# Kernel optimization log

Hardware: AMD Instinct MI355X
Metric: run time of the kernel (lower is better)

Reference implementation:

```python
import jax, jax.numpy as jnp
import numpy as np

B = 16384      # rays
H = 128        # field hidden dim


def setup_inputs() -> dict:
    key = jax.random.key(0)
    ks = jax.random.split(key, 8)
    origins = jax.random.normal(ks[0], (B, 3), dtype=jnp.float32)
    directions = jax.random.normal(ks[1], (B, 3), dtype=jnp.float32)
    directions = directions / jnp.linalg.norm(directions, axis=-1, keepdims=True)
    # Field: simple MLP 3 -> H -> H -> 4 (rgb + sigma)
    W1 = jax.random.normal(ks[2], (3, H), dtype=jnp.float32) * (1.0 / np.sqrt(3.0))
    b1 = jnp.zeros((H,), dtype=jnp.float32)
    W2 = jax.random.normal(ks[3], (H, H), dtype=jnp.float32) * (1.0 / np.sqrt(H))
    b2 = jnp.zeros((H,), dtype=jnp.float32)
    W3 = jax.random.normal(ks[4], (H, 4), dtype=jnp.float32) * (1.0 / np.sqrt(H))
    b3 = jnp.zeros((4,), dtype=jnp.float32)
    return {"origins": origins, "directions": directions,
            "W1": W1, "b1": b1, "W2": W2, "b2": b2, "W3": W3, "b3": b3,
            "near": 2, "far": 6, "num_samples": 64}


def _field(x, W1, b1, W2, b2, W3, b3):
    h = jax.nn.relu(x @ W1 + b1)
    h = jax.nn.relu(h @ W2 + b2)
    return h @ W3 + b3


def reference(origins, directions, W1, b1, W2, b2, W3, b3, near, far, num_samples):
    near = jnp.float32(near)
    far = jnp.float32(far)
    # 1. generate_samples: segment boundaries + midpoints along each ray
    depths = jnp.linspace(near, far, num_samples + 1)            # [S+1]
    midpoints = 0.5 * (depths[:-1] + depths[1:])                 # [S]
    # [B, S, 3] = origin + t * direction
    locs = origins[:, None, :] + midpoints[None, :, None] * directions[:, None, :]
    # 2. evaluate field
    f = _field(locs.reshape(-1, 3), W1, b1, W2, b2, W3, b3)
    f = f.reshape(origins.shape[0], num_samples, 4)
    # NOTE: source overwrites the sigmoid'd colors with raw outputs (faithful)
    colors = f[..., :3]                                          # [B, S, 3]
    sigma = f[..., 3]                                            # [B, S]
    # 3. alpha values
    delta = depths[1:] - depths[:-1]                             # [S]
    alphas = 1.0 - jnp.exp(-sigma * delta[None, :])              # [B, S]
    # 4. alpha compositing (black background)
    ones = jnp.ones_like(alphas[:, :1])
    transmittance = jnp.cumprod(jnp.concatenate([ones, 1.0 - alphas], axis=1), axis=1)[:, :-1]
    weights = alphas * transmittance                             # [B, S]
    radiance = jnp.sum(weights[..., None] * colors, axis=1)      # [B, 3]
    return radiance
```

## Files before the change

### kernel.cpp

```cpp
#include <hip/hip_runtime.h>


typedef _Float16 f16;
typedef __attribute__((ext_vector_type(2))) _Float16 h2v;
typedef __attribute__((ext_vector_type(8))) _Float16 half8;
typedef __attribute__((ext_vector_type(4))) float floatx4;

#define H 128
#define NS 64

static __device__ __forceinline__ h2v pkrtz(float a, float b) {
  return __builtin_bit_cast(h2v, __builtin_amdgcn_cvt_pkrtz(a, b));
}

__global__ void nerf_setup(const float* __restrict__ W2, const float* __restrict__ W3,
                           const float* __restrict__ b2,
                           f16* __restrict__ wsW2, f16* __restrict__ wsW3,
                           f16* __restrict__ wsB2) {
  int t = blockIdx.x * blockDim.x + threadIdx.x;
  if (t < 8192) {
    int j2 = t & 3, lane = (t >> 2) & 63, mt = (t >> 8) & 7, ks = t >> 11;
    int l16 = lane & 15;
    int k = ks * 32 + ((lane >> 4) * 8) + 2 * j2;
    int n = 32 * (l16 >> 2) + mt * 4 + (l16 & 3);
    wsW2[2 * t]     = (f16)W2[k * H + n];
    wsW2[2 * t + 1] = (f16)W2[(k + 1) * H + n];
  } else if (t < 9216) {
    int u = t - 8192;
    int j2 = u & 3, lane = (u >> 2) & 63, ks = u >> 8;
    int c = lane & 15;
    int k3 = 32 * (lane >> 4) + ks * 8 + 2 * j2;
    wsW3[2 * u]     = (c < 4) ? (f16)W3[k3 * 4 + c]       : (f16)0.0f;
    wsW3[2 * u + 1] = (c < 4) ? (f16)W3[(k3 + 1) * 4 + c] : (f16)0.0f;
  } else if (t < 9344) {
    int i = t - 9216;
    wsB2[i] = (f16)b2[i];
  }
}

__global__ __launch_bounds__(256, 2) void nerf_main(
    const float* __restrict__ origins, const float* __restrict__ dirs,
    const float* __restrict__ W1, const float* __restrict__ b1,
    const float* __restrict__ b3,
    const f16* __restrict__ wsW2, const f16* __restrict__ wsW3,
    const f16* __restrict__ wsB2,
    float* __restrict__ out)
{
  __shared__ __align__(16) f16   popd[4][2][H];
  __shared__ __align__(16) float f_lds[4][64][4];

  const int t = threadIdx.x;
  const int w = t >> 6, lane = t & 63, quad = lane >> 4, l16 = lane & 15;
  const float delta = 4.0f / NS;
  const int ray = blockIdx.x * 4 + w;

  {
    const float o0 = origins[ray*3], o1 = origins[ray*3+1], o2 = origins[ray*3+2];
    const float d0 = dirs[ray*3],    d1 = dirs[ray*3+1],    d2 = dirs[ray*3+2];
    const int k0 = lane * 2;
    const float2 wr0 = *(const float2*)&W1[0*H + k0];
    const float2 wr1 = *(const float2*)&W1[1*H + k0];
    const float2 wr2 = *(const float2*)&W1[2*H + k0];
    const float2 bb  = *(const float2*)&b1[k0];
    float poa = fmaf(o2, wr2.x, fmaf(o1, wr1.x, fmaf(o0, wr0.x, bb.x)));
    float pob = fmaf(o2, wr2.y, fmaf(o1, wr1.y, fmaf(o0, wr0.y, bb.y)));
    float pda = fmaf(d2, wr2.x, fmaf(d1, wr1.x, d0 * wr0.x));
    float pdb = fmaf(d2, wr2.y, fmaf(d1, wr1.y, d0 * wr0.y));
    h2v po2; po2[0] = (f16)poa; po2[1] = (f16)pob;
    h2v pd2; pd2[0] = (f16)pda; pd2[1] = (f16)pdb;
    *(h2v*)&popd[w][0][k0] = po2;
    *(h2v*)&popd[w][1][k0] = pd2;
  }

  half8 m8[4];
  #pragma unroll
  for (int tr = 0; tr < 4; ++tr)
    m8[tr] = (half8)(f16)(2.0f + (tr*16 + l16 + 0.5f) * delta);

  floatx4 acc[8][4];
  #pragma unroll
  for (int mt = 0; mt < 8; ++mt)
    #pragma unroll
    for (int tr = 0; tr < 4; ++tr) acc[mt][tr] = (floatx4)(0.0f);

  const half8* w2f = (const half8*)wsW2;
  const half8 z8 = (half8)(f16)0.0f;
  half8 awA[8], awB[8];
  #pragma unroll
  for (int mt = 0; mt < 8; ++mt) awA[mt] = w2f[mt*64 + lane];

  #pragma unroll
  for (int ks = 0; ks < 4; ++ks) {
    half8* cur = (ks & 1) ? awB : awA;
    half8* nxt = (ks & 1) ? awA : awB;
    if (ks < 3) {
      #pragma unroll
      for (int mt = 0; mt < 8; ++mt) nxt[mt] = w2f[((ks+1)*8 + mt)*64 + lane];
    }
    const half8 po8 = *(const half8*)&popd[w][0][ks*32 + quad*8];
    const half8 pd8 = *(const half8*)&popd[w][1][ks*32 + quad*8];
    #pragma unroll
    for (int tr = 0; tr < 4; ++tr) {
      half8 hb = pd8 * m8[tr] + po8;
      hb = __builtin_elementwise_max(hb, z8);
      #pragma unroll
      for (int mt = 0; mt < 8; ++mt)
        acc[mt][tr] = __builtin_amdgcn_mfma_f32_16x16x32_f16(cur[mt], hb, acc[mt][tr], 0, 0, 0);
    }
  }

  h2v bk0[8], bk1[8];
  {
    const uint2* bp = (const uint2*)wsB2;
    #pragma unroll
    for (int mt = 0; mt < 8; ++mt) {
      uint2 u = bp[quad * 8 + mt];
      bk0[mt] = __builtin_bit_cast(h2v, u.x);
      bk1[mt] = __builtin_bit_cast(h2v, u.y);
    }
  }
  const half8* w3f = (const half8*)wsW3;
  half8 w3[4];
  #pragma unroll
  for (int ks = 0; ks < 4; ++ks) w3[ks] = w3f[ks*64 + lane];

  const h2v z2 = (h2v)(f16)0.0f;
  floatx4 acc3[4];
  #pragma unroll
  for (int tr = 0; tr < 4; ++tr) {
    acc3[tr] = (floatx4)(0.0f);
    #pragma unroll
    for (int ks = 0; ks < 4; ++ks) {
      const int mt0 = 2*ks, mt1 = 2*ks + 1;
      h2v c0 = __builtin_elementwise_max((h2v)(pkrtz(acc[mt0][tr][0], acc[mt0][tr][1]) + bk0[mt0]), z2);
      h2v c1 = __builtin_elementwise_max((h2v)(pkrtz(acc[mt0][tr][2], acc[mt0][tr][3]) + bk1[mt0]), z2);
      h2v c2 = __builtin_elementwise_max((h2v)(pkrtz(acc[mt1][tr][0], acc[mt1][tr][1]) + bk0[mt1]), z2);
      h2v c3 = __builtin_elementwise_max((h2v)(pkrtz(acc[mt1][tr][2], acc[mt1][tr][3]) + bk1[mt1]), z2);
      half8 b = { c0[0], c0[1], c1[0], c1[1], c2[0], c2[1], c3[0], c3[1] };
      acc3[tr] = __builtin_amdgcn_mfma_f32_16x16x32_f16(w3[ks], b, acc3[tr], 0, 0, 0);
    }
  }

  if (quad == 0) {
    #pragma unroll
    for (int tr = 0; tr < 4; ++tr) {
      float4 fv;
      fv.x = acc3[tr][0] + b3[0];
      fv.y = acc3[tr][1] + b3[1];
      fv.z = acc3[tr][2] + b3[2];
      fv.w = acc3[tr][3] + b3[3];
      *(float4*)&f_lds[w][tr*16 + l16][0] = fv;
    }
  }

  {
    const float4 fv = *(const float4*)&f_lds[w][lane][0];
    const float sigma = fv.w;
    const float alpha = 1.0f - __expf(-sigma * delta);
    float S = sigma;
    #pragma unroll
    for (int off = 1; off < 64; off <<= 1) {
      float u = __shfl_up(S, off);
      if (lane >= off) S += u;
    }
    const float T  = __expf(-delta * (S - sigma));
    const float wt = alpha * T;
    float cr = wt * fv.x, cg = wt * fv.y, cb = wt * fv.z;
    #pragma unroll
    for (int off = 32; off > 0; off >>= 1) {
      cr += __shfl_down(cr, off);
      cg += __shfl_down(cg, off);
      cb += __shfl_down(cb, off);
    }
    if (lane == 0) {
      out[ray*3+0] = cr; out[ray*3+1] = cg; out[ray*3+2] = cb;
    }
  }
}

extern "C" void kernel_launch(void* const* d_in, const int* in_sizes, int n_in,
                              void* d_out, int out_size, void* d_ws, size_t ws_size,
                              hipStream_t stream) {
  const float* origins = (const float*)d_in[0];
  const float* dirs    = (const float*)d_in[1];
  const float* W1      = (const float*)d_in[2];
  const float* b1      = (const float*)d_in[3];
  const float* W2      = (const float*)d_in[4];
  const float* b2      = (const float*)d_in[5];
  const float* W3      = (const float*)d_in[6];
  const float* b3      = (const float*)d_in[7];
  float* out = (float*)d_out;

  f16* wsW2 = (f16*)d_ws;
  f16* wsW3 = wsW2 + 16384;
  f16* wsB2 = wsW3 + 2048;

  nerf_setup<<<37, 256, 0, stream>>>(W2, W3, b2, wsW2, wsW3, wsB2);
  nerf_main<<<16384 / 4, 256, 0, stream>>>(
      origins, dirs, W1, b1, b3, wsW2, wsW3, wsB2, out);
}
```

Baseline: 107.7 us.

## Restructure layer-2/3 MFMA loop to cut register pressure and use DPP scans

Layer 2 is now computed in slices of two output tiles at a time. Each slice feeds layer 3 immediately instead of holding all 8x4 accumulators, and the occupancy target rises from 2 to 3 blocks per CU. Biases b2 and b3 are folded into the accumulator initial values in fp32, which drops the fp16 bias conversion from setup. The shuffle-based scan and reduction are replaced with DPP inclusive scans. The trade-off is that W2 fragments are reloaded per slice without prefetch, which may expose memory latency, and a non-unrolled loop is added.

```diff
diff --git a/kernel.cpp b/kernel.cpp
--- a/kernel.cpp
+++ b/kernel.cpp
@@ -13,10 +13,25 @@
   return __builtin_bit_cast(h2v, __builtin_amdgcn_cvt_pkrtz(a, b));
 }
 
+template <int CTRL, int RM>
+static __device__ __forceinline__ float dpp_add(float x) {
+  int sh = __builtin_amdgcn_update_dpp(0, __builtin_bit_cast(int, x),
+                                       CTRL, RM, 0xf, false);
+  return x + __builtin_bit_cast(float, sh);
+}
+
+static __device__ __forceinline__ float wave_iscan(float x) {
+  x = dpp_add<0x111, 0xf>(x);
+  x = dpp_add<0x112, 0xf>(x);
+  x = dpp_add<0x114, 0xf>(x);
+  x = dpp_add<0x118, 0xf>(x);
+  x = dpp_add<0x142, 0xa>(x);
+  x = dpp_add<0x143, 0xc>(x);
+  return x;
+}
+
 __global__ void nerf_setup(const float* __restrict__ W2, const float* __restrict__ W3,
-                           const float* __restrict__ b2,
-                           f16* __restrict__ wsW2, f16* __restrict__ wsW3,
-                           f16* __restrict__ wsB2) {
+                           f16* __restrict__ wsW2, f16* __restrict__ wsW3) {
   int t = blockIdx.x * blockDim.x + threadIdx.x;
   if (t < 8192) {
     int j2 = t & 3, lane = (t >> 2) & 63, mt = (t >> 8) & 7, ks = t >> 11;
@@ -32,18 +47,14 @@
     int k3 = 32 * (lane >> 4) + ks * 8 + 2 * j2;
     wsW3[2 * u]     = (c < 4) ? (f16)W3[k3 * 4 + c]       : (f16)0.0f;
     wsW3[2 * u + 1] = (c < 4) ? (f16)W3[(k3 + 1) * 4 + c] : (f16)0.0f;
-  } else if (t < 9344) {
-    int i = t - 9216;
-    wsB2[i] = (f16)b2[i];
   }
 }
 
-__global__ __launch_bounds__(256, 2) void nerf_main(
+__global__ __launch_bounds__(256, 3) void nerf_main(
     const float* __restrict__ origins, const float* __restrict__ dirs,
     const float* __restrict__ W1, const float* __restrict__ b1,
-    const float* __restrict__ b3,
+    const float* __restrict__ b2, const float* __restrict__ b3,
     const f16* __restrict__ wsW2, const f16* __restrict__ wsW3,
-    const f16* __restrict__ wsB2,
     float* __restrict__ out)
 {
   __shared__ __align__(16) f16   popd[4][2][H];
@@ -72,72 +83,67 @@
     *(h2v*)&popd[w][1][k0] = pd2;
   }
 
-  half8 m8[4];
-  #pragma unroll
-  for (int tr = 0; tr < 4; ++tr)
-    m8[tr] = (half8)(f16)(2.0f + (tr*16 + l16 + 0.5f) * delta);
-
-  floatx4 acc[8][4];
-  #pragma unroll
-  for (int mt = 0; mt < 8; ++mt)
+  half8 hb[4][4];
+  {
+    const half8 z8 = (half8)(f16)0.0f;
+    half8 m8[4];
     #pragma unroll
-    for (int tr = 0; tr < 4; ++tr) acc[mt][tr] = (floatx4)(0.0f);
-
-  const half8* w2f = (const half8*)wsW2;
-  const half8 z8 = (half8)(f16)0.0f;
-  half8 awA[8], awB[8];
-  #pragma unroll
-  for (int mt = 0; mt < 8; ++mt) awA[mt] = w2f[mt*64 + lane];
-
-  #pragma unroll
-  for (int ks = 0; ks < 4; ++ks) {
-    half8* cur = (ks & 1) ? awB : awA;
-    half8* nxt = (ks & 1) ? awA : awB;
-    if (ks < 3) {
+    for (int tr = 0; tr < 4; ++tr)
+      m8[tr] = (half8)(f16)(2.0f + (tr*16 + l16 + 0.5f) * delta);
+    #pragma unroll
+    for (int ks = 0; ks < 4; ++ks) {
+      const half8 po8 = *(const half8*)&popd[w][0][ks*32 + quad*8];
+      const half8 pd8 = *(const half8*)&popd[w][1][ks*32 + quad*8];
       #pragma unroll
-      for (int mt = 0; mt < 8; ++mt) nxt[mt] = w2f[((ks+1)*8 + mt)*64 + lane];
-    }
-    const half8 po8 = *(const half8*)&popd[w][0][ks*32 + quad*8];
-    const half8 pd8 = *(const half8*)&popd[w][1][ks*32 + quad*8];
-    #pragma unroll
-    for (int tr = 0; tr < 4; ++tr) {
-      half8 hb = pd8 * m8[tr] + po8;
-      hb = __builtin_elementwise_max(hb, z8);
-      #pragma unroll
-      for (int mt = 0; mt < 8; ++mt)
-        acc[mt][tr] = __builtin_amdgcn_mfma_f32_16x16x32_f16(cur[mt], hb, acc[mt][tr], 0, 0, 0);
+      for (int tr = 0; tr < 4; ++tr)
+        hb[ks][tr] = __builtin_elementwise_max(pd8 * m8[tr] + po8, z8);
     }
   }
 
-  h2v bk0[8], bk1[8];
+  const half8* w2f = (const half8*)wsW2;
+  const half8* w3f = (const half8*)wsW3;
+  const h2v z2 = (h2v)(f16)0.0f;
+
+  floatx4 acc3[4];
   {
-    const uint2* bp = (const uint2*)wsB2;
+    const float4 b3v = *(const float4*)&b3[0];
     #pragma unroll
-    for (int mt = 0; mt < 8; ++mt) {
-      uint2 u = bp[quad * 8 + mt];
-      bk0[mt] = __builtin_bit_cast(h2v, u.x);
-      bk1[mt] = __builtin_bit_cast(h2v, u.y);
+    for (int tr = 0; tr < 4; ++tr) {
+      acc3[tr][0] = b3v.x; acc3[tr][1] = b3v.y;
+      acc3[tr][2] = b3v.z; acc3[tr][3] = b3v.w;
     }
   }
-  const half8* w3f = (const half8*)wsW3;
-  half8 w3[4];
-  #pragma unroll
-  for (int ks = 0; ks < 4; ++ks) w3[ks] = w3f[ks*64 + lane];
 
-  const h2v z2 = (h2v)(f16)0.0f;
-  floatx4 acc3[4];
-  #pragma unroll
-  for (int tr = 0; tr < 4; ++tr) {
-    acc3[tr] = (floatx4)(0.0f);
+  #pragma unroll 1
+  for (int ks3 = 0; ks3 < 4; ++ks3) {
+    const int mt0 = 2 * ks3, mt1 = mt0 + 1;
+    const float4 bA = *(const float4*)&b2[quad*32 + mt0*4];
+    const float4 bB = *(const float4*)&b2[quad*32 + mt1*4];
+    const half8 w3k = w3f[ks3*64 + lane];
+    floatx4 accA[4], accB[4];
     #pragma unroll
-    for (int ks = 0; ks < 4; ++ks) {
-      const int mt0 = 2*ks, mt1 = 2*ks + 1;
-      h2v c0 = __builtin_elementwise_max((h2v)(pkrtz(acc[mt0][tr][0], acc[mt0][tr][1]) + bk0[mt0]), z2);
-      h2v c1 = __builtin_elementwise_max((h2v)(pkrtz(acc[mt0][tr][2], acc[mt0][tr][3]) + bk1[mt0]), z2);
-      h2v c2 = __builtin_elementwise_max((h2v)(pkrtz(acc[mt1][tr][0], acc[mt1][tr][1]) + bk0[mt1]), z2);
-      h2v c3 = __builtin_elementwise_max((h2v)(pkrtz(acc[mt1][tr][2], acc[mt1][tr][3]) + bk1[mt1]), z2);
+    for (int tr = 0; tr < 4; ++tr) {
+      accA[tr][0] = bA.x; accA[tr][1] = bA.y; accA[tr][2] = bA.z; accA[tr][3] = bA.w;
+      accB[tr][0] = bB.x; accB[tr][1] = bB.y; accB[tr][2] = bB.z; accB[tr][3] = bB.w;
+    }
+    #pragma unroll
+    for (int ks2 = 0; ks2 < 4; ++ks2) {
+      const half8 wA = w2f[(ks2*8 + mt0)*64 + lane];
+      const half8 wB = w2f[(ks2*8 + mt1)*64 + lane];
+      #pragma unroll
+      for (int tr = 0; tr < 4; ++tr) {
+        accA[tr] = __builtin_amdgcn_mfma_f32_16x16x32_f16(wA, hb[ks2][tr], accA[tr], 0, 0, 0);
+        accB[tr] = __builtin_amdgcn_mfma_f32_16x16x32_f16(wB, hb[ks2][tr], accB[tr], 0, 0, 0);
+      }
+    }
+    #pragma unroll
+    for (int tr = 0; tr < 4; ++tr) {
+      h2v c0 = __builtin_elementwise_max(pkrtz(accA[tr][0], accA[tr][1]), z2);
+      h2v c1 = __builtin_elementwise_max(pkrtz(accA[tr][2], accA[tr][3]), z2);
+      h2v c2 = __builtin_elementwise_max(pkrtz(accB[tr][0], accB[tr][1]), z2);
+      h2v c3 = __builtin_elementwise_max(pkrtz(accB[tr][2], accB[tr][3]), z2);
       half8 b = { c0[0], c0[1], c1[0], c1[1], c2[0], c2[1], c3[0], c3[1] };
-      acc3[tr] = __builtin_amdgcn_mfma_f32_16x16x32_f16(w3[ks], b, acc3[tr], 0, 0, 0);
+      acc3[tr] = __builtin_amdgcn_mfma_f32_16x16x32_f16(w3k, b, acc3[tr], 0, 0, 0);
     }
   }
 
@@ -145,10 +151,8 @@
     #pragma unroll
     for (int tr = 0; tr < 4; ++tr) {
       float4 fv;
-      fv.x = acc3[tr][0] + b3[0];
-      fv.y = acc3[tr][1] + b3[1];
-      fv.z = acc3[tr][2] + b3[2];
-      fv.w = acc3[tr][3] + b3[3];
+      fv.x = acc3[tr][0]; fv.y = acc3[tr][1];
+      fv.z = acc3[tr][2]; fv.w = acc3[tr][3];
       *(float4*)&f_lds[w][tr*16 + l16][0] = fv;
     }
   }
@@ -157,23 +161,14 @@
     const float4 fv = *(const float4*)&f_lds[w][lane][0];
     const float sigma = fv.w;
     const float alpha = 1.0f - __expf(-sigma * delta);
-    float S = sigma;
-    #pragma unroll
-    for (int off = 1; off < 64; off <<= 1) {
-      float u = __shfl_up(S, off);
-      if (lane >= off) S += u;
-    }
+    const float S  = wave_iscan(sigma);
     const float T  = __expf(-delta * (S - sigma));
     const float wt = alpha * T;
-    float cr = wt * fv.x, cg = wt * fv.y, cb = wt * fv.z;
-    #pragma unroll
-    for (int off = 32; off > 0; off >>= 1) {
-      cr += __shfl_down(cr, off);
-      cg += __shfl_down(cg, off);
-      cb += __shfl_down(cb, off);
-    }
-    if (lane == 0) {
-      out[ray*3+0] = cr; out[ray*3+1] = cg; out[ray*3+2] = cb;
+    const float sr = wave_iscan(wt * fv.x);
+    const float sg = wave_iscan(wt * fv.y);
+    const float sb = wave_iscan(wt * fv.z);
+    if (lane == 63) {
+      out[ray*3+0] = sr; out[ray*3+1] = sg; out[ray*3+2] = sb;
     }
   }
 }
@@ -193,9 +188,8 @@
 
   f16* wsW2 = (f16*)d_ws;
   f16* wsW3 = wsW2 + 16384;
-  f16* wsB2 = wsW3 + 2048;
 
-  nerf_setup<<<37, 256, 0, stream>>>(W2, W3, b2, wsW2, wsW3, wsB2);
+  nerf_setup<<<36, 256, 0, stream>>>(W2, W3, wsW2, wsW3);
   nerf_main<<<16384 / 4, 256, 0, stream>>>(
-      origins, dirs, W1, b1, b3, wsW2, wsW3, wsB2, out);
+      origins, dirs, W1, b1, b2, b3, wsW2, wsW3, out);
 }
```

Measured after the change: 106.3 us. Within noise of the previous version (-1.3%).
